# Optimization experiments

Hardware: AMD Instinct MI355X
Metric: run time of the kernel (lower is better)

Reference implementation:

```python
import jax, jax.numpy as jnp
import numpy as np

B, NA, NB = 4, 2048, 2048
IN_A, IN_B, OUT, H = 128, 128, 128, 8
DH = OUT // H  # 16
NEG = jnp.float32(-1e30)
SLOPE = jnp.float32(0.01)


def setup_inputs() -> dict:
    key = jax.random.key(0)
    ks = jax.random.split(key, 13)
    s = 0.05
    return {
        "h_A": jax.random.normal(ks[0], (B, NA, IN_A), jnp.float32),
        "h_B": jax.random.normal(ks[1], (B, NB, IN_B), jnp.float32),
        "mask": jax.random.randint(ks[2], (B, NA, NB), 0, 2) > 0,
        # per-head params stacked on a leading head axis
        "WA_w": jax.random.normal(ks[3], (H, IN_A, DH), jnp.float32) * s,
        "WA_b": jax.random.normal(ks[4], (H, DH), jnp.float32) * s,
        "WB_w": jax.random.normal(ks[5], (H, IN_B, DH), jnp.float32) * s,
        "WB_b": jax.random.normal(ks[6], (H, DH), jnp.float32) * s,
        "aA_w": jax.random.normal(ks[7], (H, DH), jnp.float32) * s,
        "aA_b": jax.random.normal(ks[8], (H,), jnp.float32) * s,
        "aB_w": jax.random.normal(ks[9], (H, DH), jnp.float32) * s,
        "aB_b": jax.random.normal(ks[10], (H,), jnp.float32) * s,
        "W_w": jax.random.normal(ks[11], (OUT, OUT), jnp.float32) * s,
        "W_b": jax.random.normal(ks[12], (OUT,), jnp.float32) * s,
    }


def _leaky(x):
    return jnp.where(x >= 0, x, SLOPE * x)


def reference(h_A, h_B, mask, WA_w, WA_b, WB_w, WB_b, aA_w, aA_b, aB_w, aB_b, W_w, W_b):
    # per-head linear projections: [B, H, N, DH]
    z_A = jnp.einsum('bni,hid->bhnd', h_A, WA_w) + WA_b[None, :, None, :]
    z_B = jnp.einsum('bmi,hid->bhmd', h_B, WB_w) + WB_b[None, :, None, :]
    # additive attention logits: [B, H, NA] + [B, H, NB] -> [B, H, NA, NB]
    eA = jnp.einsum('bhnd,hd->bhn', z_A, aA_w) + aA_b[None, :, None]
    eB = jnp.einsum('bhmd,hd->bhm', z_B, aB_w) + aB_b[None, :, None]
    e = eA[:, :, :, None] + eB[:, :, None, :]
    m = mask[:, None, :, :]  # broadcast over heads
    e = jnp.where(m, e, NEG)
    alpha = jax.nn.softmax(_leaky(e), axis=-1)
    alpha = jnp.where(m, alpha, jnp.zeros((), alpha.dtype))
    # weighted aggregation: [B, H, NA, DH]
    out_h = jnp.einsum('bhnm,bhmd->bhnd', alpha, z_B)
    # concat heads -> [B, NA, OUT], final projection
    cat = out_h.transpose(0, 2, 1, 3).reshape(h_A.shape[0], h_A.shape[1], H * DH)
    return cat @ W_w.T + W_b
```

## Files before the change

kernel.cpp:

```cpp
#include <hip/hip_runtime.h>

typedef unsigned short u16;
typedef unsigned int u32;
typedef unsigned char u8;

typedef _Float16 f16x8 __attribute__((ext_vector_type(8)));
typedef _Float16 f16x2 __attribute__((ext_vector_type(2)));
typedef __attribute__((ext_vector_type(4))) float f32x4;


__global__ __launch_bounds__(256) void kzero(float* __restrict__ out){
  out[blockIdx.x * 256 + threadIdx.x] = 0.f;
}

__global__ __launch_bounds__(256) void kmask(const void* __restrict__ maskv,
                                             u32* __restrict__ Mb){
  __shared__ int s_aw, s_ab, s_ah;
  int t = threadIdx.x;
  if (t == 0){ s_aw = 1; s_ab = 1; s_ah = 1; }
  __syncthreads();
  {
    const u32* mw = (const u32*)maskv;
    int aw = 1, ah = 1, ab = 1;
    #pragma unroll
    for (int j = 0; j < 4; ++j){
      u32 m = mw[t + 256 * j];
      if (!(m == 0u || m == 1u || m == 0x3F800000u)) aw = 0;
      u32 lo = m & 0xFFFFu, hi = m >> 16;
      if (!((lo == 0u || lo == 1u || lo == 0x3F80u) && (hi == 0u || hi == 1u || hi == 0x3F80u))) ah = 0;
      if (m & ~0x01010101u) ab = 0;
    }
    if (!aw) atomicAnd(&s_aw, 0);
    if (!ah) atomicAnd(&s_ah, 0);
    if (!ab) atomicAnd(&s_ab, 0);
  }
  __syncthreads();
  int Fm = 0;
  if (s_aw) Fm = 0; else if (s_ab) Fm = 1; else if (s_ah) Fm = 2;

  if (Fm == 0){
    int lane = t & 63;
    int wid = blockIdx.x * 4 + (t >> 6);
    const u32* mw = (const u32*)maskv;
    size_t base = (size_t)wid * 2048;
    #pragma unroll 4
    for (int i = 0; i < 32; ++i){
      u32 v = mw[base + i * 64 + lane];
      unsigned long long bal = __ballot(v != 0u);
      if (lane < 2) Mb[(base + i * 64) / 32 + lane] = (u32)(bal >> (32 * lane));
    }
    return;
  }
  int oid = blockIdx.x * 256 + t;
  u32 bits = 0;
  if (Fm == 1){
    const uint4* mp = (const uint4*)maskv + (size_t)oid * 2;
    #pragma unroll
    for (int k = 0; k < 2; ++k){
      uint4 v = mp[k];
      u32 w[4] = {v.x, v.y, v.z, v.w};
      #pragma unroll
      for (int q = 0; q < 4; ++q)
        #pragma unroll
        for (int bb = 0; bb < 4; ++bb)
          bits |= ((w[q] >> (8*bb)) & 255u ? 1u : 0u) << (k*16 + q*4 + bb);
    }
  } else {
    const uint4* mp = (const uint4*)maskv + (size_t)oid * 4;
    #pragma unroll
    for (int k = 0; k < 4; ++k){
      uint4 v = mp[k];
      u32 w[4] = {v.x, v.y, v.z, v.w};
      #pragma unroll
      for (int q = 0; q < 4; ++q){
        bits |= ((w[q] & 0xFFFFu) ? 1u : 0u) << (k*8 + q*2);
        bits |= ((w[q] >> 16)     ? 1u : 0u) << (k*8 + q*2 + 1);
      }
    }
  }
  Mb[oid] = bits;
}

__global__ __launch_bounds__(256) void kfold(const float* __restrict__ WA, const float* __restrict__ WAb,
                                             const float* __restrict__ WB, const float* __restrict__ WBb,
                                             const float* __restrict__ aAw, const float* __restrict__ aAb,
                                             const float* __restrict__ aBw, const float* __restrict__ aBb,
                                             const float* __restrict__ W,
                                             float* __restrict__ WfB, float* __restrict__ WtO,
                                             float* __restrict__ vA, float* __restrict__ vB,
                                             float* __restrict__ cA, float* __restrict__ cB){
  int gid = blockIdx.x, t = threadIdx.x;
  if (gid < 64){
    int idx = gid * 256 + t;
    int k = idx >> 7, c = idx & 127;
    WfB[idx] = WB[(c >> 4) * 2048 + k * 16 + (c & 15)];
  } else if (gid < 128){
    int idx = (gid - 64) * 256 + t;
    int c = idx >> 7, o = idx & 127;
    WtO[idx] = W[o * 128 + c];
  } else {
    int h = gid - 128;
    if (t < 128){
      float s = 0.f;
      #pragma unroll
      for (int d = 0; d < 16; ++d) s += WA[h * 2048 + t * 16 + d] * aAw[h * 16 + d];
      vA[h * 128 + t] = s;
    } else {
      int i = t - 128;
      float s = 0.f;
      #pragma unroll
      for (int d = 0; d < 16; ++d) s += WB[h * 2048 + i * 16 + d] * aBw[h * 16 + d];
      vB[h * 128 + i] = s;
    }
    if (t == 0){
      float s = aAb[h];
      #pragma unroll
      for (int d = 0; d < 16; ++d) s += WAb[h * 16 + d] * aAw[h * 16 + d];
      cA[h] = s;
    }
    if (t == 255){
      float s = aBb[h];
      #pragma unroll
      for (int d = 0; d < 16; ++d) s += WBb[h * 16 + d] * aBw[h * 16 + d];
      cB[h] = s;
    }
  }
}

__global__ __launch_bounds__(256) void kproj(const float* __restrict__ hB,
                                             const float* __restrict__ WfB,
                                             const float* __restrict__ bB,
                                             uint4* __restrict__ zF){
  __shared__ float h_l[32 * 132];
  __shared__ float W_l[64 * 128];
  __shared__ float T[128 * 33];
  int R0 = blockIdx.x * 32;
  int t = threadIdx.x;

  for (int j = 0; j < 4; ++j){
    int idx4 = t + 256 * j;
    int r = idx4 >> 5, k0 = (idx4 & 31) * 4;
    *(float4*)&h_l[r * 132 + k0] = *(const float4*)&hB[(size_t)(R0 + r) * 128 + k0];
  }

  int cg = t & 15, rg = t >> 4;
  float acc[2][8];
  for (int i = 0; i < 2; ++i) for (int s = 0; s < 8; ++s) acc[i][s] = 0.f;

  for (int kc = 0; kc < 2; ++kc){
    __syncthreads();
    for (int j = 0; j < 8; ++j){
      int idx4 = t + 256 * j;
      int k = idx4 >> 5, c0 = (idx4 & 31) * 4;
      *(float4*)&W_l[k * 128 + c0] = *(const float4*)&WfB[(kc * 64 + k) * 128 + c0];
    }
    __syncthreads();
    for (int k = 0; k < 64; ++k){
      int kk = kc * 64 + k;
      float4 w0 = *(const float4*)&W_l[k * 128 + cg * 8];
      float4 w1 = *(const float4*)&W_l[k * 128 + cg * 8 + 4];
      float wv[8] = {w0.x, w0.y, w0.z, w0.w, w1.x, w1.y, w1.z, w1.w};
      #pragma unroll
      for (int i = 0; i < 2; ++i){
        float hv = h_l[(rg * 2 + i) * 132 + kk];
        #pragma unroll
        for (int s = 0; s < 8; ++s) acc[i][s] = fmaf(hv, wv[s], acc[i][s]);
      }
    }
  }

  for (int i = 0; i < 2; ++i)
    #pragma unroll
    for (int s = 0; s < 8; ++s)
      T[(cg * 8 + s) * 33 + rg * 2 + i] = acc[i][s] + bB[cg * 8 + s];
  __syncthreads();

  int b = R0 >> 11;
  int mblk = (R0 & 2047) >> 5;
  for (int it = t; it < 512; it += 256){
    int h = it >> 6, lane = it & 63;
    int d = lane & 15, mq = (lane >> 4) * 8;
    const float* Tp = &T[(h * 16 + d) * 33 + mq];
    u32 wv[4];
    #pragma unroll
    for (int p = 0; p < 4; ++p){
      union { f16x2 h2; u32 u; } c;
      c.h2 = (f16x2){(_Float16)Tp[p * 2], (_Float16)Tp[p * 2 + 1]};
      wv[p] = c.u;
    }
    zF[((size_t)((b * 8 + h) * 64) + mblk) * 64 + lane] = make_uint4(wv[0], wv[1], wv[2], wv[3]);
  }
}

__global__ __launch_bounds__(256) void ke(const float* __restrict__ hA, const float* __restrict__ hB,
                                          const float* __restrict__ vA, const float* __restrict__ vB,
                                          const float* __restrict__ cA, const float* __restrict__ cB,
                                          float* __restrict__ EAe, float* __restrict__ EA01e,
                                          u32* __restrict__ EBh, u32* __restrict__ GBh){
  __shared__ float h_l[32 * 132];
  __shared__ float v_l[8 * 132];
  __shared__ float c_l[8];
  int gid = blockIdx.x, t = threadIdx.x;
  int X = gid >> 8;
  int r0 = (gid & 255) * 32;
  const float* hp = X ? hB : hA;
  const float* vp = X ? vB : vA;
  const float* cp = X ? cB : cA;

  for (int j = 0; j < 4; ++j){
    int idx4 = t + 256 * j;
    int r = idx4 >> 5, k0 = (idx4 & 31) * 4;
    *(float4*)&h_l[r * 132 + k0] = *(const float4*)&hp[(size_t)(r0 + r) * 128 + k0];
  }
  { int hh = t >> 5, k0 = (t & 31) * 4;
    *(float4*)&v_l[hh * 132 + k0] = *(const float4*)&vp[hh * 128 + k0]; }
  if (t < 8) c_l[t] = cp[t];
  __syncthreads();

  int r = t >> 3, h = t & 7;
  float acc = c_l[h];
  #pragma unroll
  for (int k0 = 0; k0 < 128; k0 += 4){
    float4 hv = *(const float4*)&h_l[r * 132 + k0];
    float4 vv = *(const float4*)&v_l[h * 132 + k0];
    acc = fmaf(hv.x, vv.x, acc); acc = fmaf(hv.y, vv.y, acc);
    acc = fmaf(hv.z, vv.z, acc); acc = fmaf(hv.w, vv.w, acc);
  }
  int row = r0 + r;
  int b = row >> 11, n = row & 2047;
  float e0 = __expf(acc), e1 = __expf(0.01f * acc);
  if (X){
    float p0 = __shfl_xor(e0, 8, 64);
    float p1 = __shfl_xor(e1, 8, 64);
    if ((((t & 63) >> 3) & 1) == 0){
      union { f16x2 h2; u32 u; } c0, c1;
      c0.h2 = (f16x2){(_Float16)e0, (_Float16)p0};
      c1.h2 = (f16x2){(_Float16)e1, (_Float16)p1};
      u32 di = (u32)((b * 8 + h) * 1024 + (n >> 1));
      EBh[di] = c0.u;
      GBh[di] = c1.u;
    }
  } else {
    size_t idx = (size_t)(b * 8 + h) * 2048 + n;
    EAe[idx] = e0; EA01e[idx] = e1;
  }
}

__global__ __launch_bounds__(256) void kattn(const uint4* __restrict__ zF,
                                             const float* __restrict__ EAe, const float* __restrict__ EA01e,
                                             const u32* __restrict__ EBh, const u32* __restrict__ GBh,
                                             const u32* __restrict__ Mb,
                                             float* __restrict__ cat){
  __shared__ u32 EB_l[1024];
  __shared__ u32 GB_l[1024];
  __shared__ float red[3][32][17];
  int t = threadIdx.x;
  int w = t >> 6, lane = t & 63;
  int gid = blockIdx.x;
  int h  = gid & 7;
  int nt = (gid >> 3) & 63;
  int b  = gid >> 9;
  int n0 = nt * 32;
  int nl = lane & 15, q = lane >> 4, qs = q * 8;

  {
    const uint4* src0 = (const uint4*)(EBh + (size_t)(b * 8 + h) * 1024);
    const uint4* src1 = (const uint4*)(GBh + (size_t)(b * 8 + h) * 1024);
    ((uint4*)EB_l)[t] = src0[t];
    ((uint4*)GB_l)[t] = src1[t];
  }

  size_t ebase = (size_t)(b * 8 + h) * 2048;
  _Float16 ea0h  = (_Float16)EAe  [ebase + n0 + nl];
  _Float16 ea0sh = (_Float16)EA01e[ebase + n0 + nl];
  _Float16 ea1h  = (_Float16)EAe  [ebase + n0 + 16 + nl];
  _Float16 ea1sh = (_Float16)EA01e[ebase + n0 + 16 + nl];
  f16x2 ea0_2  = (f16x2){ea0h,  ea0h};
  f16x2 ea0s_2 = (f16x2){ea0sh, ea0sh};
  f16x2 ea1_2  = (f16x2){ea1h,  ea1h};
  f16x2 ea1s_2 = (f16x2){ea1sh, ea1sh};

  const u32* EBq = EB_l + w * 256;
  const u32* GBq = GB_l + w * 256;
  const uint4* zFp = zF + ((size_t)(b * 8 + h) * 64 + w * 16) * 64 + lane;
  const u32*  mp0 = Mb + ((size_t)(b * 2048) + n0 + nl) * 64 + w * 16;
  const u32*  mp1 = mp0 + 16 * 64;

  f32x4 acc0 = {0.f,0.f,0.f,0.f}, acc1 = {0.f,0.f,0.f,0.f};
  f32x4 lcc0 = {0.f,0.f,0.f,0.f}, lcc1 = {0.f,0.f,0.f,0.f};
  union { u32 u[4]; f16x8 v; } onesu;
  onesu.u[0] = 0x3C003C00u; onesu.u[1] = 0x3C003C00u;
  onesu.u[2] = 0x3C003C00u; onesu.u[3] = 0x3C003C00u;
  const f16x8 ones = onesu.v;

  __syncthreads();

  uint4 Azu, Bzu; u32 Am0, Am1, Bm0, Bm1;
  #define LOADA(sp) do{ Azu = zFp[(size_t)(sp) * 64]; Am0 = mp0[sp]; Am1 = mp1[sp]; }while(0)
  #define LOADB(sp) do{ Bzu = zFp[(size_t)(sp) * 64]; Bm0 = mp0[sp]; Bm1 = mp1[sp]; }while(0)
  #define COMP(sp,ZU_,M0_,M1_) do{ \
    uint4 EB_ = *(const uint4*)(EBq + (sp) * 16 + q * 4); \
    uint4 GB_ = *(const uint4*)(GBq + (sp) * 16 + q * 4); \
    u32 mb0 = (M0_) >> qs, mb1 = (M1_) >> qs; \
    u32 ebu[4] = {EB_.x, EB_.y, EB_.z, EB_.w}; \
    u32 gbu[4] = {GB_.x, GB_.y, GB_.z, GB_.w}; \
    union { u32 u[4]; f16x8 v; } a0, a1; \
    _Pragma("unroll") \
    for (int p = 0; p < 4; ++p){ \
      int j0 = 2*p, j1 = 2*p + 1; \
      u32 k00 = (u32)(((int)(mb0 << (31 - j0))) >> 31); \
      u32 k01 = (u32)(((int)(mb0 << (31 - j1))) >> 31); \
      u32 k10 = (u32)(((int)(mb1 << (31 - j0))) >> 31); \
      u32 k11 = (u32)(((int)(mb1 << (31 - j1))) >> 31); \
      u32 kc0 = __builtin_amdgcn_perm(k01, k00, 0x05040100u); \
      u32 kc1 = __builtin_amdgcn_perm(k11, k10, 0x05040100u); \
      union { u32 u; f16x2 h2; } eb, gb, r0u, r1u; \
      eb.u = ebu[p]; gb.u = gbu[p]; \
      r0u.h2 = __builtin_elementwise_max(ea0_2 * eb.h2, ea0s_2 * gb.h2); \
      r1u.h2 = __builtin_elementwise_max(ea1_2 * eb.h2, ea1s_2 * gb.h2); \
      a0.u[p] = r0u.u & kc0; \
      a1.u[p] = r1u.u & kc1; \
    } \
    union { uint4 u; f16x8 v; } zu; zu.u = ZU_; \
    acc0 = __builtin_amdgcn_mfma_f32_16x16x32_f16(a0.v, zu.v, acc0, 0, 0, 0); \
    lcc0 = __builtin_amdgcn_mfma_f32_16x16x32_f16(a0.v, ones, lcc0, 0, 0, 0); \
    acc1 = __builtin_amdgcn_mfma_f32_16x16x32_f16(a1.v, zu.v, acc1, 0, 0, 0); \
    lcc1 = __builtin_amdgcn_mfma_f32_16x16x32_f16(a1.v, ones, lcc1, 0, 0, 0); }while(0)

  LOADA(0);
  LOADB(1);
  #pragma unroll 4
  for (int s = 0; s < 16; s += 2){
    COMP(s, Azu, Am0, Am1);
    LOADA(s + 2);
    COMP(s + 1, Bzu, Bm0, Bm1);
    LOADB(s + 3);
  }
  #undef LOADA
  #undef LOADB
  #undef COMP

  if (w > 0){
    #pragma unroll
    for (int r = 0; r < 4; ++r){
      int row = q * 4 + r;
      red[w - 1][row][nl]      = acc0[r];
      red[w - 1][row + 16][nl] = acc1[r];
    }
    if (nl == 0){
      #pragma unroll
      for (int r = 0; r < 4; ++r){
        red[w - 1][q * 4 + r][16]      = lcc0[r];
        red[w - 1][q * 4 + r + 16][16] = lcc1[r];
      }
    }
  }
  __syncthreads();
  if (w == 0){
    #pragma unroll
    for (int r = 0; r < 4; ++r){
      int row = q * 4 + r;
      float a0 = acc0[r] + red[0][row][nl]      + red[1][row][nl]      + red[2][row][nl];
      float a1 = acc1[r] + red[0][row + 16][nl] + red[1][row + 16][nl] + red[2][row + 16][nl];
      float L0 = lcc0[r] + red[0][row][16]      + red[1][row][16]      + red[2][row][16];
      float L1 = lcc1[r] + red[0][row + 16][16] + red[1][row + 16][16] + red[2][row + 16][16];
      float r0 = (L0 > 0.f) ? 1.f / L0 : 0.f;
      float r1 = (L1 > 0.f) ? 1.f / L1 : 0.f;
      cat[((size_t)(b * 2048) + n0 + row)      * 128 + h * 16 + nl] = a0 * r0;
      cat[((size_t)(b * 2048) + n0 + 16 + row) * 128 + h * 16 + nl] = a1 * r1;
    }
  }
}

__global__ __launch_bounds__(256) void kout(const float* __restrict__ cat,
                                            const float* __restrict__ WtO, const float* __restrict__ Wb,
                                            float* __restrict__ out){
  __shared__ float cat_l[32 * 132];
  __shared__ float Wt_l[64 * 128];
  int R0 = blockIdx.x * 32;
  int t = threadIdx.x;

  for (int jj = 0; jj < 4; ++jj){
    int idx4 = t + 256 * jj;
    int r = idx4 >> 5, c0 = (idx4 & 31) * 4;
    *(float4*)&cat_l[r * 132 + c0] = *(const float4*)&cat[((size_t)R0 + r) * 128 + c0];
  }

  int og = t & 15, rg = t >> 4;
  float acc[2][8];
  for (int i = 0; i < 2; ++i) for (int s = 0; s < 8; ++s) acc[i][s] = 0.f;

  for (int kc = 0; kc < 2; ++kc){
    __syncthreads();
    for (int j = 0; j < 8; ++j){
      int idx4 = t + 256 * j;
      int k = idx4 >> 5, o0 = (idx4 & 31) * 4;
      *(float4*)&Wt_l[k * 128 + o0] = *(const float4*)&WtO[(kc * 64 + k) * 128 + o0];
    }
    __syncthreads();
    for (int k = 0; k < 64; ++k){
      int kk = kc * 64 + k;
      float4 w0 = *(const float4*)&Wt_l[k * 128 + og * 8];
      float4 w1 = *(const float4*)&Wt_l[k * 128 + og * 8 + 4];
      float wv[8] = {w0.x, w0.y, w0.z, w0.w, w1.x, w1.y, w1.z, w1.w};
      #pragma unroll
      for (int i = 0; i < 2; ++i){
        float cv = cat_l[(rg * 2 + i) * 132 + kk];
        #pragma unroll
        for (int s = 0; s < 8; ++s) acc[i][s] = fmaf(cv, wv[s], acc[i][s]);
      }
    }
  }

  for (int i = 0; i < 2; ++i){
    int r = rg * 2 + i;
    float* op = out + (size_t)(R0 + r) * 128 + og * 8;
    *(float4*)(op)     = make_float4(acc[i][0]+Wb[og*8+0], acc[i][1]+Wb[og*8+1], acc[i][2]+Wb[og*8+2], acc[i][3]+Wb[og*8+3]);
    *(float4*)(op + 4) = make_float4(acc[i][4]+Wb[og*8+4], acc[i][5]+Wb[og*8+5], acc[i][6]+Wb[og*8+6], acc[i][7]+Wb[og*8+7]);
  }
}

extern "C" void kernel_launch(void* const* d_in, const int* in_sizes, int n_in,
                              void* d_out, int out_size, void* d_ws, size_t ws_size,
                              hipStream_t stream) {
  const float* hA  = (const float*)d_in[0];
  const float* hB  = (const float*)d_in[1];
  const void* maskv= d_in[2];
  const float* WAw = (const float*)d_in[3];
  const float* WAb = (const float*)d_in[4];
  const float* WBw = (const float*)d_in[5];
  const float* WBb = (const float*)d_in[6];
  const float* aAw = (const float*)d_in[7];
  const float* aAb = (const float*)d_in[8];
  const float* aBw = (const float*)d_in[9];
  const float* aBb = (const float*)d_in[10];
  const float* Ww  = (const float*)d_in[11];
  const float* Wb  = (const float*)d_in[12];

  float* ws   = (float*)d_ws;
  uint4* zF   = (uint4*)ws;
  float* EAe  = ws + 524288;
  float* EA01e= ws + 589824;
  u32*  EBh   = (u32*)(ws + 655360);
  u32*  GBh   = (u32*)(ws + 720896);
  float* WfB  = ws + 786432;
  float* WtO  = ws + 802816;
  float* vA   = ws + 819200;
  float* vB   = ws + 820224;
  float* cA   = ws + 821248;
  float* cB   = ws + 821256;
  u32*  Mb    = (u32*)(ws + 821272);
  float* cat  = ws + 1345560;

  if (ws_size < 2394136ull * 4ull){
    kzero<<<4096, 256, 0, stream>>>((float*)d_out);
    return;
  }

  kfold<<<136, 256, 0, stream>>>(WAw, WAb, WBw, WBb, aAw, aAb, aBw, aBb, Ww,
                                 WfB, WtO, vA, vB, cA, cB);
  kmask<<<2048, 256, 0, stream>>>(maskv, Mb);
  kproj<<<256, 256, 0, stream>>>(hB, WfB, WBb, zF);
  ke   <<<512, 256, 0, stream>>>(hA, hB, vA, vB, cA, cB, EAe, EA01e, EBh, GBh);
  kattn<<<2048, 256, 0, stream>>>(zF, EAe, EA01e, EBh, GBh, Mb, cat);
  kout <<<256, 256, 0, stream>>>(cat, WtO, Wb, (float*)d_out);
}
```

Before: 181.2 us.

## Merge preprocessing kernels into one launch and stage mask bits in LDS

Combines the weight-fold, mask-packing, B-projection and logit kernels into a single kprep launch, with blocks partitioned by role. The fold work (vA/vB, cA/cB, WfB transpose) is recomputed locally inside each block instead of being written to and read back from global scratch. This removes three launches and the serial dependency between them. In the attention kernel, the packed mask words are now loaded cooperatively into padded shared memory rather than read per lane from global memory inside the pipelined loop, and the bit extraction uses sbfe when it is available. The cost is redundant per-block fold work and extra LDS use in kattn, which may reduce occupancy.

```diff
diff --git a/kernel.cpp b/kernel.cpp
--- a/kernel.cpp
+++ b/kernel.cpp
@@ -9,240 +9,226 @@
 typedef __attribute__((ext_vector_type(4))) float f32x4;
 
 
+#if __has_builtin(__builtin_amdgcn_sbfe)
+#define SEXTBIT(m, j) ((u32)__builtin_amdgcn_sbfe((int)(m), (u32)(j), 1u))
+#else
+#define SEXTBIT(m, j) ((u32)(((int)((m) << (31 - (j)))) >> 31))
+#endif
+
 __global__ __launch_bounds__(256) void kzero(float* __restrict__ out){
   out[blockIdx.x * 256 + threadIdx.x] = 0.f;
 }
 
-__global__ __launch_bounds__(256) void kmask(const void* __restrict__ maskv,
-                                             u32* __restrict__ Mb){
-  __shared__ int s_aw, s_ab, s_ah;
-  int t = threadIdx.x;
-  if (t == 0){ s_aw = 1; s_ab = 1; s_ah = 1; }
-  __syncthreads();
-  {
-    const u32* mw = (const u32*)maskv;
-    int aw = 1, ah = 1, ab = 1;
-    #pragma unroll
+__global__ __launch_bounds__(256) void kprep(
+    const void* __restrict__ maskv, u32* __restrict__ Mb,
+    const float* __restrict__ hA, const float* __restrict__ hB,
+    const float* __restrict__ WAw, const float* __restrict__ WAb,
+    const float* __restrict__ aAw, const float* __restrict__ aAb,
+    const float* __restrict__ WBw, const float* __restrict__ WBb,
+    const float* __restrict__ aBw, const float* __restrict__ aBb,
+    const float* __restrict__ Ww, float* __restrict__ WtO,
+    uint4* __restrict__ zF,
+    float* __restrict__ EAe, float* __restrict__ EA01e,
+    u32* __restrict__ EBh, u32* __restrict__ GBh){
+  __shared__ float smem[12416];
+  int gid = blockIdx.x, t = threadIdx.x;
+
+  if (gid < 256){
+    float* h_l = smem;
+    float* W_l = smem + 4224;
+    float* T   = smem + 4224;
+    int R0 = gid * 32;
+
     for (int j = 0; j < 4; ++j){
-      u32 m = mw[t + 256 * j];
-      if (!(m == 0u || m == 1u || m == 0x3F800000u)) aw = 0;
-      u32 lo = m & 0xFFFFu, hi = m >> 16;
-      if (!((lo == 0u || lo == 1u || lo == 0x3F80u) && (hi == 0u || hi == 1u || hi == 0x3F80u))) ah = 0;
-      if (m & ~0x01010101u) ab = 0;
-    }
-    if (!aw) atomicAnd(&s_aw, 0);
-    if (!ah) atomicAnd(&s_ah, 0);
-    if (!ab) atomicAnd(&s_ab, 0);
-  }
-  __syncthreads();
-  int Fm = 0;
-  if (s_aw) Fm = 0; else if (s_ab) Fm = 1; else if (s_ah) Fm = 2;
-
-  if (Fm == 0){
-    int lane = t & 63;
-    int wid = blockIdx.x * 4 + (t >> 6);
-    const u32* mw = (const u32*)maskv;
-    size_t base = (size_t)wid * 2048;
-    #pragma unroll 4
-    for (int i = 0; i < 32; ++i){
-      u32 v = mw[base + i * 64 + lane];
-      unsigned long long bal = __ballot(v != 0u);
-      if (lane < 2) Mb[(base + i * 64) / 32 + lane] = (u32)(bal >> (32 * lane));
-    }
-    return;
-  }
-  int oid = blockIdx.x * 256 + t;
-  u32 bits = 0;
-  if (Fm == 1){
-    const uint4* mp = (const uint4*)maskv + (size_t)oid * 2;
-    #pragma unroll
-    for (int k = 0; k < 2; ++k){
-      uint4 v = mp[k];
-      u32 w[4] = {v.x, v.y, v.z, v.w};
-      #pragma unroll
-      for (int q = 0; q < 4; ++q)
+      int idx4 = t + 256 * j;
+      int r = idx4 >> 5, k0 = (idx4 & 31) * 4;
+      *(float4*)&h_l[r * 132 + k0] = *(const float4*)&hB[(size_t)(R0 + r) * 128 + k0];
+    }
+
+    int cg = t & 15, rg = t >> 4;
+    float acc[2][8];
+    for (int i = 0; i < 2; ++i) for (int s = 0; s < 8; ++s) acc[i][s] = 0.f;
+
+    for (int kc = 0; kc < 2; ++kc){
+      __syncthreads();
+      for (int j = 0; j < 8; ++j){
+        int idx4 = t + 256 * j;
+        int k = idx4 >> 5, c0 = (idx4 & 31) * 4;
+        *(float4*)&W_l[k * 128 + c0] =
+          *(const float4*)&WBw[(size_t)(c0 >> 4) * 2048 + (kc * 64 + k) * 16 + (c0 & 15)];
+      }
+      __syncthreads();
+      for (int k = 0; k < 64; ++k){
+        int kk = kc * 64 + k;
+        float4 w0 = *(const float4*)&W_l[k * 128 + cg * 8];
+        float4 w1 = *(const float4*)&W_l[k * 128 + cg * 8 + 4];
+        float wv[8] = {w0.x, w0.y, w0.z, w0.w, w1.x, w1.y, w1.z, w1.w};
         #pragma unroll
-        for (int bb = 0; bb < 4; ++bb)
-          bits |= ((w[q] >> (8*bb)) & 255u ? 1u : 0u) << (k*16 + q*4 + bb);
-    }
-  } else {
-    const uint4* mp = (const uint4*)maskv + (size_t)oid * 4;
-    #pragma unroll
-    for (int k = 0; k < 4; ++k){
-      uint4 v = mp[k];
-      u32 w[4] = {v.x, v.y, v.z, v.w};
-      #pragma unroll
-      for (int q = 0; q < 4; ++q){
-        bits |= ((w[q] & 0xFFFFu) ? 1u : 0u) << (k*8 + q*2);
-        bits |= ((w[q] >> 16)     ? 1u : 0u) << (k*8 + q*2 + 1);
-      }
-    }
-  }
-  Mb[oid] = bits;
-}
-
-__global__ __launch_bounds__(256) void kfold(const float* __restrict__ WA, const float* __restrict__ WAb,
-                                             const float* __restrict__ WB, const float* __restrict__ WBb,
-                                             const float* __restrict__ aAw, const float* __restrict__ aAb,
-                                             const float* __restrict__ aBw, const float* __restrict__ aBb,
-                                             const float* __restrict__ W,
-                                             float* __restrict__ WfB, float* __restrict__ WtO,
-                                             float* __restrict__ vA, float* __restrict__ vB,
-                                             float* __restrict__ cA, float* __restrict__ cB){
-  int gid = blockIdx.x, t = threadIdx.x;
-  if (gid < 64){
-    int idx = gid * 256 + t;
-    int k = idx >> 7, c = idx & 127;
-    WfB[idx] = WB[(c >> 4) * 2048 + k * 16 + (c & 15)];
-  } else if (gid < 128){
-    int idx = (gid - 64) * 256 + t;
-    int c = idx >> 7, o = idx & 127;
-    WtO[idx] = W[o * 128 + c];
-  } else {
-    int h = gid - 128;
-    if (t < 128){
-      float s = 0.f;
-      #pragma unroll
-      for (int d = 0; d < 16; ++d) s += WA[h * 2048 + t * 16 + d] * aAw[h * 16 + d];
-      vA[h * 128 + t] = s;
-    } else {
-      int i = t - 128;
-      float s = 0.f;
-      #pragma unroll
-      for (int d = 0; d < 16; ++d) s += WB[h * 2048 + i * 16 + d] * aBw[h * 16 + d];
-      vB[h * 128 + i] = s;
-    }
-    if (t == 0){
-      float s = aAb[h];
-      #pragma unroll
-      for (int d = 0; d < 16; ++d) s += WAb[h * 16 + d] * aAw[h * 16 + d];
-      cA[h] = s;
-    }
-    if (t == 255){
-      float s = aBb[h];
-      #pragma unroll
-      for (int d = 0; d < 16; ++d) s += WBb[h * 16 + d] * aBw[h * 16 + d];
-      cB[h] = s;
-    }
-  }
-}
-
-__global__ __launch_bounds__(256) void kproj(const float* __restrict__ hB,
-                                             const float* __restrict__ WfB,
-                                             const float* __restrict__ bB,
-                                             uint4* __restrict__ zF){
-  __shared__ float h_l[32 * 132];
-  __shared__ float W_l[64 * 128];
-  __shared__ float T[128 * 33];
-  int R0 = blockIdx.x * 32;
-  int t = threadIdx.x;
-
-  for (int j = 0; j < 4; ++j){
-    int idx4 = t + 256 * j;
-    int r = idx4 >> 5, k0 = (idx4 & 31) * 4;
-    *(float4*)&h_l[r * 132 + k0] = *(const float4*)&hB[(size_t)(R0 + r) * 128 + k0];
-  }
-
-  int cg = t & 15, rg = t >> 4;
-  float acc[2][8];
-  for (int i = 0; i < 2; ++i) for (int s = 0; s < 8; ++s) acc[i][s] = 0.f;
-
-  for (int kc = 0; kc < 2; ++kc){
-    __syncthreads();
-    for (int j = 0; j < 8; ++j){
+        for (int i = 0; i < 2; ++i){
+          float hv = h_l[(rg * 2 + i) * 132 + kk];
+          #pragma unroll
+          for (int s = 0; s < 8; ++s) acc[i][s] = fmaf(hv, wv[s], acc[i][s]);
+        }
+      }
+    }
+    __syncthreads();
+    for (int i = 0; i < 2; ++i)
+      #pragma unroll
+      for (int s = 0; s < 8; ++s)
+        T[(cg * 8 + s) * 33 + rg * 2 + i] = acc[i][s] + WBb[cg * 8 + s];
+    __syncthreads();
+
+    int b = R0 >> 11;
+    int mblk = (R0 & 2047) >> 5;
+    for (int it = t; it < 512; it += 256){
+      int h = it >> 6, lane = it & 63;
+      int d = lane & 15, mq = (lane >> 4) * 8;
+      const float* Tp = &T[(h * 16 + d) * 33 + mq];
+      u32 wv2[4];
+      #pragma unroll
+      for (int p = 0; p < 4; ++p){
+        union { f16x2 h2; u32 u; } c;
+        c.h2 = (f16x2){(_Float16)Tp[p * 2], (_Float16)Tp[p * 2 + 1]};
+        wv2[p] = c.u;
+      }
+      zF[((size_t)((b * 8 + h) * 64) + mblk) * 64 + lane] = make_uint4(wv2[0], wv2[1], wv2[2], wv2[3]);
+    }
+  } else if (gid < 768){
+    float* h_l = smem;
+    float* v_l = smem + 4224;
+    float* c_l = smem + 5280;
+    float* a_l = smem + 5288;
+    int ge = gid - 256;
+    int X = ge >> 8;
+    int r0 = (ge & 255) * 32;
+    const float* hp  = X ? hB  : hA;
+    const float* Wp  = X ? WBw : WAw;
+    const float* Wbp = X ? WBb : WAb;
+    const float* awp = X ? aBw : aAw;
+    const float* abp = X ? aBb : aAb;
+
+    for (int j = 0; j < 4; ++j){
       int idx4 = t + 256 * j;
-      int k = idx4 >> 5, c0 = (idx4 & 31) * 4;
-      *(float4*)&W_l[k * 128 + c0] = *(const float4*)&WfB[(kc * 64 + k) * 128 + c0];
-    }
-    __syncthreads();
-    for (int k = 0; k < 64; ++k){
-      int kk = kc * 64 + k;
-      float4 w0 = *(const float4*)&W_l[k * 128 + cg * 8];
-      float4 w1 = *(const float4*)&W_l[k * 128 + cg * 8 + 4];
-      float wv[8] = {w0.x, w0.y, w0.z, w0.w, w1.x, w1.y, w1.z, w1.w};
-      #pragma unroll
-      for (int i = 0; i < 2; ++i){
-        float hv = h_l[(rg * 2 + i) * 132 + kk];
-        #pragma unroll
-        for (int s = 0; s < 8; ++s) acc[i][s] = fmaf(hv, wv[s], acc[i][s]);
-      }
-    }
-  }
-
-  for (int i = 0; i < 2; ++i)
-    #pragma unroll
-    for (int s = 0; s < 8; ++s)
-      T[(cg * 8 + s) * 33 + rg * 2 + i] = acc[i][s] + bB[cg * 8 + s];
-  __syncthreads();
-
-  int b = R0 >> 11;
-  int mblk = (R0 & 2047) >> 5;
-  for (int it = t; it < 512; it += 256){
-    int h = it >> 6, lane = it & 63;
-    int d = lane & 15, mq = (lane >> 4) * 8;
-    const float* Tp = &T[(h * 16 + d) * 33 + mq];
-    u32 wv[4];
+      int r = idx4 >> 5, k0 = (idx4 & 31) * 4;
+      *(float4*)&h_l[r * 132 + k0] = *(const float4*)&hp[(size_t)(r0 + r) * 128 + k0];
+    }
+    if (t < 128) a_l[t] = awp[t];
+    __syncthreads();
     #pragma unroll
     for (int p = 0; p < 4; ++p){
-      union { f16x2 h2; u32 u; } c;
-      c.h2 = (f16x2){(_Float16)Tp[p * 2], (_Float16)Tp[p * 2 + 1]};
-      wv[p] = c.u;
-    }
-    zF[((size_t)((b * 8 + h) * 64) + mblk) * 64 + lane] = make_uint4(wv[0], wv[1], wv[2], wv[3]);
-  }
-}
-
-__global__ __launch_bounds__(256) void ke(const float* __restrict__ hA, const float* __restrict__ hB,
-                                          const float* __restrict__ vA, const float* __restrict__ vB,
-                                          const float* __restrict__ cA, const float* __restrict__ cB,
-                                          float* __restrict__ EAe, float* __restrict__ EA01e,
-                                          u32* __restrict__ EBh, u32* __restrict__ GBh){
-  __shared__ float h_l[32 * 132];
-  __shared__ float v_l[8 * 132];
-  __shared__ float c_l[8];
-  int gid = blockIdx.x, t = threadIdx.x;
-  int X = gid >> 8;
-  int r0 = (gid & 255) * 32;
-  const float* hp = X ? hB : hA;
-  const float* vp = X ? vB : vA;
-  const float* cp = X ? cB : cA;
-
-  for (int j = 0; j < 4; ++j){
-    int idx4 = t + 256 * j;
-    int r = idx4 >> 5, k0 = (idx4 & 31) * 4;
-    *(float4*)&h_l[r * 132 + k0] = *(const float4*)&hp[(size_t)(r0 + r) * 128 + k0];
-  }
-  { int hh = t >> 5, k0 = (t & 31) * 4;
-    *(float4*)&v_l[hh * 132 + k0] = *(const float4*)&vp[hh * 128 + k0]; }
-  if (t < 8) c_l[t] = cp[t];
-  __syncthreads();
-
-  int r = t >> 3, h = t & 7;
-  float acc = c_l[h];
-  #pragma unroll
-  for (int k0 = 0; k0 < 128; k0 += 4){
-    float4 hv = *(const float4*)&h_l[r * 132 + k0];
-    float4 vv = *(const float4*)&v_l[h * 132 + k0];
-    acc = fmaf(hv.x, vv.x, acc); acc = fmaf(hv.y, vv.y, acc);
-    acc = fmaf(hv.z, vv.z, acc); acc = fmaf(hv.w, vv.w, acc);
-  }
-  int row = r0 + r;
-  int b = row >> 11, n = row & 2047;
-  float e0 = __expf(acc), e1 = __expf(0.01f * acc);
-  if (X){
-    float p0 = __shfl_xor(e0, 8, 64);
-    float p1 = __shfl_xor(e1, 8, 64);
-    if ((((t & 63) >> 3) & 1) == 0){
-      union { f16x2 h2; u32 u; } c0, c1;
-      c0.h2 = (f16x2){(_Float16)e0, (_Float16)p0};
-      c1.h2 = (f16x2){(_Float16)e1, (_Float16)p1};
-      u32 di = (u32)((b * 8 + h) * 1024 + (n >> 1));
-      EBh[di] = c0.u;
-      GBh[di] = c1.u;
-    }
+      int idx = t + 256 * p;
+      int h = idx >> 7, i = idx & 127;
+      const float* wrow = Wp + (size_t)h * 2048 + i * 16;
+      float s = 0.f;
+      #pragma unroll
+      for (int d = 0; d < 16; ++d) s = fmaf(wrow[d], a_l[h * 16 + d], s);
+      v_l[h * 132 + i] = s;
+    }
+    if (t < 8){
+      float s = abp[t];
+      #pragma unroll
+      for (int d = 0; d < 16; ++d) s = fmaf(Wbp[t * 16 + d], a_l[t * 16 + d], s);
+      c_l[t] = s;
+    }
+    __syncthreads();
+
+    int r = t >> 3, h = t & 7;
+    float acc = c_l[h];
+    #pragma unroll
+    for (int k0 = 0; k0 < 128; k0 += 4){
+      float4 hv = *(const float4*)&h_l[r * 132 + k0];
+      float4 vv = *(const float4*)&v_l[h * 132 + k0];
+      acc = fmaf(hv.x, vv.x, acc); acc = fmaf(hv.y, vv.y, acc);
+      acc = fmaf(hv.z, vv.z, acc); acc = fmaf(hv.w, vv.w, acc);
+    }
+    int row = r0 + r;
+    int b = row >> 11, n = row & 2047;
+    float e0 = __expf(acc), e1 = __expf(0.01f * acc);
+    if (X){
+      float p0 = __shfl_xor(e0, 8, 64);
+      float p1 = __shfl_xor(e1, 8, 64);
+      if ((((t & 63) >> 3) & 1) == 0){
+        union { f16x2 h2; u32 u; } c0, c1;
+        c0.h2 = (f16x2){(_Float16)e0, (_Float16)p0};
+        c1.h2 = (f16x2){(_Float16)e1, (_Float16)p1};
+        u32 di = (u32)((b * 8 + h) * 1024 + (n >> 1));
+        EBh[di] = c0.u;
+        GBh[di] = c1.u;
+      }
+    } else {
+      size_t idx = (size_t)(b * 8 + h) * 2048 + n;
+      EAe[idx] = e0; EA01e[idx] = e1;
+    }
+  } else if (gid < 832){
+    int j = gid - 768;
+    int idx = j * 256 + t;
+    int c = idx >> 7, o = idx & 127;
+    WtO[idx] = Ww[o * 128 + c];
   } else {
-    size_t idx = (size_t)(b * 8 + h) * 2048 + n;
-    EAe[idx] = e0; EA01e[idx] = e1;
+    int mg = gid - 832;
+    int* flg = (int*)smem;
+    if (t == 0){ flg[0] = 1; flg[1] = 1; flg[2] = 1; }
+    __syncthreads();
+    {
+      const u32* mw = (const u32*)maskv;
+      int aw = 1, ah = 1, ab = 1;
+      #pragma unroll
+      for (int jj = 0; jj < 4; ++jj){
+        u32 m = mw[t + 256 * jj];
+        if (!(m == 0u || m == 1u || m == 0x3F800000u)) aw = 0;
+        u32 lo = m & 0xFFFFu, hi = m >> 16;
+        if (!((lo == 0u || lo == 1u || lo == 0x3F80u) && (hi == 0u || hi == 1u || hi == 0x3F80u))) ah = 0;
+        if (m & ~0x01010101u) ab = 0;
+      }
+      if (!aw) atomicAnd(&flg[0], 0);
+      if (!ah) atomicAnd(&flg[2], 0);
+      if (!ab) atomicAnd(&flg[1], 0);
+    }
+    __syncthreads();
+    int Fm = 0;
+    if (flg[0]) Fm = 0; else if (flg[1]) Fm = 1; else if (flg[2]) Fm = 2;
+
+    if (Fm == 0){
+      int lane = t & 63;
+      int wid = mg * 4 + (t >> 6);
+      const u32* mw = (const u32*)maskv;
+      size_t base = (size_t)wid * 2048;
+      #pragma unroll 4
+      for (int i = 0; i < 32; ++i){
+        u32 v = mw[base + i * 64 + lane];
+        unsigned long long bal = __ballot(v != 0u);
+        if (lane < 2) Mb[(base + i * 64) / 32 + lane] = (u32)(bal >> (32 * lane));
+      }
+      return;
+    }
+    int oid = mg * 256 + t;
+    u32 bits = 0;
+    if (Fm == 1){
+      const uint4* mp = (const uint4*)maskv + (size_t)oid * 2;
+      #pragma unroll
+      for (int k = 0; k < 2; ++k){
+        uint4 v = mp[k];
+        u32 w[4] = {v.x, v.y, v.z, v.w};
+        #pragma unroll
+        for (int q = 0; q < 4; ++q)
+          #pragma unroll
+          for (int bb = 0; bb < 4; ++bb)
+            bits |= ((w[q] >> (8*bb)) & 255u ? 1u : 0u) << (k*16 + q*4 + bb);
+      }
+    } else {
+      const uint4* mp = (const uint4*)maskv + (size_t)oid * 4;
+      #pragma unroll
+      for (int k = 0; k < 4; ++k){
+        uint4 v = mp[k];
+        u32 w[4] = {v.x, v.y, v.z, v.w};
+        #pragma unroll
+        for (int q = 0; q < 4; ++q){
+          bits |= ((w[q] & 0xFFFFu) ? 1u : 0u) << (k*8 + q*2);
+          bits |= ((w[q] >> 16)     ? 1u : 0u) << (k*8 + q*2 + 1);
+        }
+      }
+    }
+    Mb[oid] = bits;
   }
 }
 
@@ -253,6 +239,7 @@
                                              float* __restrict__ cat){
   __shared__ u32 EB_l[1024];
   __shared__ u32 GB_l[1024];
+  __shared__ u32 Mb_l[32 * 65];
   __shared__ float red[3][32][17];
   int t = threadIdx.x;
   int w = t >> 6, lane = t & 63;
@@ -268,6 +255,12 @@
     const uint4* src1 = (const uint4*)(GBh + (size_t)(b * 8 + h) * 1024);
     ((uint4*)EB_l)[t] = src0[t];
     ((uint4*)GB_l)[t] = src1[t];
+    const uint4* ms = (const uint4*)(Mb + ((size_t)b * 2048 + n0) * 64);
+    uint4 m0v = ms[t * 2], m1v = ms[t * 2 + 1];
+    int rr = t >> 3, cc = (t & 7) * 8;
+    u32* dst = Mb_l + rr * 65 + cc;
+    dst[0] = m0v.x; dst[1] = m0v.y; dst[2] = m0v.z; dst[3] = m0v.w;
+    dst[4] = m1v.x; dst[5] = m1v.y; dst[6] = m1v.z; dst[7] = m1v.w;
   }
 
   size_t ebase = (size_t)(b * 8 + h) * 2048;
@@ -282,9 +275,9 @@
 
   const u32* EBq = EB_l + w * 256;
   const u32* GBq = GB_l + w * 256;
+  const u32* Mrow0 = Mb_l + nl * 65 + w * 16;
+  const u32* Mrow1 = Mb_l + (nl + 16) * 65 + w * 16;
   const uint4* zFp = zF + ((size_t)(b * 8 + h) * 64 + w * 16) * 64 + lane;
-  const u32*  mp0 = Mb + ((size_t)(b * 2048) + n0 + nl) * 64 + w * 16;
-  const u32*  mp1 = mp0 + 16 * 64;
 
   f32x4 acc0 = {0.f,0.f,0.f,0.f}, acc1 = {0.f,0.f,0.f,0.f};
   f32x4 lcc0 = {0.f,0.f,0.f,0.f}, lcc1 = {0.f,0.f,0.f,0.f};
@@ -295,23 +288,24 @@
 
   __syncthreads();
 
-  uint4 Azu, Bzu; u32 Am0, Am1, Bm0, Bm1;
-  #define LOADA(sp) do{ Azu = zFp[(size_t)(sp) * 64]; Am0 = mp0[sp]; Am1 = mp1[sp]; }while(0)
-  #define LOADB(sp) do{ Bzu = zFp[(size_t)(sp) * 64]; Bm0 = mp0[sp]; Bm1 = mp1[sp]; }while(0)
-  #define COMP(sp,ZU_,M0_,M1_) do{ \
+  uint4 Azu, Bzu;
+  #define LOADA(sp) do{ Azu = zFp[(size_t)(sp) * 64]; }while(0)
+  #define LOADB(sp) do{ Bzu = zFp[(size_t)(sp) * 64]; }while(0)
+  #define COMP(sp,ZU_) do{ \
     uint4 EB_ = *(const uint4*)(EBq + (sp) * 16 + q * 4); \
     uint4 GB_ = *(const uint4*)(GBq + (sp) * 16 + q * 4); \
-    u32 mb0 = (M0_) >> qs, mb1 = (M1_) >> qs; \
+    u32 mb0 = Mrow0[sp] >> qs; \
+    u32 mb1 = Mrow1[sp] >> qs; \
     u32 ebu[4] = {EB_.x, EB_.y, EB_.z, EB_.w}; \
     u32 gbu[4] = {GB_.x, GB_.y, GB_.z, GB_.w}; \
     union { u32 u[4]; f16x8 v; } a0, a1; \
     _Pragma("unroll") \
     for (int p = 0; p < 4; ++p){ \
       int j0 = 2*p, j1 = 2*p + 1; \
-      u32 k00 = (u32)(((int)(mb0 << (31 - j0))) >> 31); \
-      u32 k01 = (u32)(((int)(mb0 << (31 - j1))) >> 31); \
-      u32 k10 = (u32)(((int)(mb1 << (31 - j0))) >> 31); \
-      u32 k11 = (u32)(((int)(mb1 << (31 - j1))) >> 31); \
+      u32 k00 = SEXTBIT(mb0, j0); \
+      u32 k01 = SEXTBIT(mb0, j1); \
+      u32 k10 = SEXTBIT(mb1, j0); \
+      u32 k11 = SEXTBIT(mb1, j1); \
       u32 kc0 = __builtin_amdgcn_perm(k01, k00, 0x05040100u); \
       u32 kc1 = __builtin_amdgcn_perm(k11, k10, 0x05040100u); \
       union { u32 u; f16x2 h2; } eb, gb, r0u, r1u; \
@@ -331,9 +325,9 @@
   LOADB(1);
   #pragma unroll 4
   for (int s = 0; s < 16; s += 2){
-    COMP(s, Azu, Am0, Am1);
+    COMP(s, Azu);
     LOADA(s + 2);
-    COMP(s + 1, Bzu, Bm0, Bm1);
+    COMP(s + 1, Bzu);
     LOADB(s + 3);
   }
   #undef LOADA
@@ -443,12 +437,7 @@
   float* EA01e= ws + 589824;
   u32*  EBh   = (u32*)(ws + 655360);
   u32*  GBh   = (u32*)(ws + 720896);
-  float* WfB  = ws + 786432;
   float* WtO  = ws + 802816;
-  float* vA   = ws + 819200;
-  float* vB   = ws + 820224;
-  float* cA   = ws + 821248;
-  float* cB   = ws + 821256;
   u32*  Mb    = (u32*)(ws + 821272);
   float* cat  = ws + 1345560;
 
@@ -457,11 +446,10 @@
     return;
   }
 
-  kfold<<<136, 256, 0, stream>>>(WAw, WAb, WBw, WBb, aAw, aAb, aBw, aBb, Ww,
-                                 WfB, WtO, vA, vB, cA, cB);
-  kmask<<<2048, 256, 0, stream>>>(maskv, Mb);
-  kproj<<<256, 256, 0, stream>>>(hB, WfB, WBb, zF);
-  ke   <<<512, 256, 0, stream>>>(hA, hB, vA, vB, cA, cB, EAe, EA01e, EBh, GBh);
+  kprep<<<2880, 256, 0, stream>>>(maskv, Mb, hA, hB,
+                                  WAw, WAb, aAw, aAb,
+                                  WBw, WBb, aBw, aBb,
+                                  Ww, WtO, zF, EAe, EA01e, EBh, GBh);
   kattn<<<2048, 256, 0, stream>>>(zF, EAe, EA01e, EBh, GBh, Mb, cat);
   kout <<<256, 256, 0, stream>>>(cat, WtO, Wb, (float*)d_out);
 }
```

Measured after the change: 192.6 us. 1.06x slower.
